# Kernel tuning notes

Measured on AMD Instinct MI355X. Metric: run time of the kernel, lower is better.

The kernel has to match this reference:

```python
import jax, jax.numpy as jnp
import numpy as np

# static multi-scale config (Deformable-DETR encoder, 1024x1024 image, strides 8/16/32/64)
SPATIAL_SHAPES = np.array([[128, 128], [64, 64], [32, 32], [16, 16]])  # (L, 2) = (h, w)
NUM_HEADS, NUM_LEVELS, NUM_POINTS = 8, 4, 4
EMBED, HEAD_DIM = 256, 32
NUM_KEYS = int(SPATIAL_SHAPES.prod(-1).sum())  # 21760


def _grid_sample(img, grid):
    """Bilinear grid_sample, padding_mode='zeros', align_corners=False.
    img: (BH, C, H, W); grid: (BH, Nq, P, 2) in [-1,1] -> (BH, C, Nq, P)."""
    BH, C, H, W = img.shape
    gx = (grid[..., 0] + 1.0) * (W / 2) - 0.5
    gy = (grid[..., 1] + 1.0) * (H / 2) - 0.5
    x0f, y0f = jnp.floor(gx), jnp.floor(gy)
    wx, wy = gx - x0f, gy - y0f
    x0, y0 = x0f.astype(jnp.int32), y0f.astype(jnp.int32)
    flat = img.reshape(BH, C, H * W)

    def gather(xi, yi, w):
        valid = (xi >= 0) & (xi < W) & (yi >= 0) & (yi < H)
        idx = jnp.clip(yi, 0, H - 1) * W + jnp.clip(xi, 0, W - 1)
        g = jnp.take_along_axis(flat, idx.reshape(BH, 1, -1), axis=2)
        g = g.reshape(BH, C, xi.shape[1], xi.shape[2])
        return g * (w * valid)[:, None]

    return (gather(x0, y0, (1 - wx) * (1 - wy)) + gather(x0 + 1, y0, wx * (1 - wy))
            + gather(x0, y0 + 1, (1 - wx) * wy) + gather(x0 + 1, y0 + 1, wx * wy))


def setup_inputs() -> dict:
    key = jax.random.key(0)
    ks = jax.random.split(key, 12)
    bs, nq = 1, NUM_KEYS
    s = 1.0 / np.sqrt(EMBED)
    return {
        "query": jax.random.normal(ks[0], (bs, nq, EMBED), jnp.float32),
        "query_pos": jax.random.normal(ks[1], (bs, nq, EMBED), jnp.float32),
        "value": jax.random.normal(ks[2], (bs, NUM_KEYS, EMBED), jnp.float32),
        "reference_points": jax.random.uniform(ks[3], (bs, nq, NUM_LEVELS, 2), jnp.float32),
        "spatial_shapes": jnp.asarray(SPATIAL_SHAPES, jnp.int32),
        "W_value": jax.random.normal(ks[4], (EMBED, EMBED), jnp.float32) * s,
        "b_value": jnp.zeros((EMBED,), jnp.float32),
        "W_off": jax.random.normal(ks[5], (NUM_HEADS * NUM_LEVELS * NUM_POINTS * 2, EMBED), jnp.float32) * 0.01,
        "b_off": jax.random.normal(ks[6], (NUM_HEADS * NUM_LEVELS * NUM_POINTS * 2,), jnp.float32),
        "W_attn": jax.random.normal(ks[7], (NUM_HEADS * NUM_LEVELS * NUM_POINTS, EMBED), jnp.float32) * s,
        "b_attn": jnp.zeros((NUM_HEADS * NUM_LEVELS * NUM_POINTS,), jnp.float32),
        "W_out": jax.random.normal(ks[8], (EMBED, EMBED), jnp.float32) * s,
        "b_out": jnp.zeros((EMBED,), jnp.float32),
    }


def reference(query, query_pos, value, reference_points, spatial_shapes,
              W_value, b_value, W_off, b_off, W_attn, b_attn, W_out, b_out):
    bs, nq, _ = query.shape
    identity = query
    q = query + query_pos  # pos_add
    v = value @ W_value.T + b_value  # value_proj: (bs, nk, E)
    v = v.reshape(bs, -1, NUM_HEADS, HEAD_DIM)

    offsets = (q @ W_off.T + b_off).reshape(bs, nq, NUM_HEADS, NUM_LEVELS, NUM_POINTS, 2)
    attn = (q @ W_attn.T + b_attn).reshape(bs, nq, NUM_HEADS, NUM_LEVELS * NUM_POINTS)
    attn = jax.nn.softmax(attn, axis=-1).reshape(bs, nq, NUM_HEADS, NUM_LEVELS, NUM_POINTS)

    # offset_normalizer = (w, h) per level; ref points are 2D -> loc = ref + off/norm
    normalizer = jnp.asarray(SPATIAL_SHAPES[:, ::-1].copy(), query.dtype)  # (L, 2)
    loc = reference_points[:, :, None, :, None, :] + offsets / normalizer[None, None, None, :, None, :]
    grids = 2.0 * loc - 1.0  # (bs, nq, H, L, P, 2)

    starts = np.concatenate([[0], np.cumsum(SPATIAL_SHAPES.prod(-1))])
    sampled = []
    for lvl in range(NUM_LEVELS):
        H_, W_ = int(SPATIAL_SHAPES[lvl, 0]), int(SPATIAL_SHAPES[lvl, 1])
        v_l = v[:, int(starts[lvl]):int(starts[lvl + 1])]  # (bs, H*W, heads, Dh)
        v_l = v_l.transpose(0, 2, 3, 1).reshape(bs * NUM_HEADS, HEAD_DIM, H_, W_)
        g_l = grids[:, :, :, lvl].transpose(0, 2, 1, 3, 4).reshape(bs * NUM_HEADS, nq, NUM_POINTS, 2)
        sampled.append(_grid_sample(v_l, g_l))  # (bs*H, Dh, nq, P)
    sampled = jnp.concatenate(sampled, axis=-1)  # (bs*H, Dh, nq, L*P)

    aw = attn.transpose(0, 2, 1, 3, 4).reshape(bs * NUM_HEADS, 1, nq, NUM_LEVELS * NUM_POINTS)
    out = (sampled * aw).sum(-1).reshape(bs, NUM_HEADS * HEAD_DIM, nq).transpose(0, 2, 1)
    out = out @ W_out.T + b_out  # output_proj
    return out + identity  # residual (dropout is identity at eval)
```

## Files before the change

kernel.cpp:

```cpp
#include <hip/hip_runtime.h>
#include <hip/hip_bf16.h>
#include <math.h>
#include <type_traits>

#define K_DIM 256
using bf16 = __hip_bfloat16;

typedef __attribute__((ext_vector_type(8))) short s8v;
typedef __attribute__((ext_vector_type(4))) float f4v;

__device__ __forceinline__ float b2f(unsigned short u) {
    return __uint_as_float(((unsigned)u) << 16);
}
__device__ __forceinline__ unsigned short f2b(float f) {
    unsigned u = __float_as_uint(f);
    unsigned r = 0x7FFFu + ((u >> 16) & 1u);
    return (unsigned short)((u + r) >> 16);
}
__device__ __forceinline__ float  ld1(const float* p) { return *p; }
__device__ __forceinline__ float  ld1(const bf16*  p) { return b2f(*(const unsigned short*)p); }
__device__ __forceinline__ void   st1(float* p, float v) { *p = v; }
__device__ __forceinline__ void   st1(bf16*  p, float v) { *(unsigned short*)p = f2b(v); }
__device__ __forceinline__ float4 ld4(const float* p) { return *(const float4*)p; }
__device__ __forceinline__ float4 ld4(const bf16*  p) {
    ushort4 u = *(const ushort4*)p;
    return make_float4(b2f(u.x), b2f(u.y), b2f(u.z), b2f(u.w));
}
__device__ __forceinline__ s8v ldw8(const bf16* p) { return *(const s8v*)p; }

__device__ __forceinline__ bool detect_bf16(const unsigned* __restrict__ qw) {
    unsigned w = qw[threadIdx.x & 63];
    unsigned t = (w >> 8) & 0x7F;
    bool hit = (t >= 0x3Bu) && (t <= 0x42u);
    unsigned long long m = __ballot(hit);
    return __popcll(m) >= 32;
}

#define P1_TOTAL 164480
__global__ __launch_bounds__(256) void k_prep1(
    const unsigned* __restrict__ qd,
    const void* wv, const void* wo, const void* wa,
    const void* bv, const void* bo, const void* ba, bf16* __restrict__ dst)
{
    const bool isb = detect_bf16(qd);
    const int i4 = (blockIdx.x * 256 + threadIdx.x) * 4;
    if (i4 >= P1_TOTAL) return;
    const void* src; int off;
    if      (i4 < 65536)  { src = wv; off = i4; }
    else if (i4 < 131072) { src = wo; off = i4 - 65536; }
    else if (i4 < 163840) { src = wa; off = i4 - 131072; }
    else if (i4 < 164096) { src = bv; off = i4 - 163840; }
    else if (i4 < 164352) { src = bo; off = i4 - 164096; }
    else                  { src = ba; off = i4 - 164352; }
    if (isb) {
        *(ushort4*)(dst + i4) = *(const ushort4*)((const unsigned short*)src + off);
    } else {
        float4 v = *(const float4*)((const float*)src + off);
        *(ushort4*)(dst + i4) = make_ushort4(f2b(v.x), f2b(v.y), f2b(v.z), f2b(v.w));
    }
}

#define P2_TOTAL 65792
__global__ __launch_bounds__(256) void k_prep2(
    const unsigned* __restrict__ qd,
    const void* wout, const void* bout, bf16* __restrict__ dst)
{
    const bool isb = detect_bf16(qd);
    const int i4 = (blockIdx.x * 256 + threadIdx.x) * 4;
    if (i4 >= P2_TOTAL) return;
    const void* src; int off;
    if (i4 < 65536) { src = wout; off = i4; }
    else            { src = bout; off = i4 - 65536; }
    if (isb) {
        *(ushort4*)(dst + i4) = *(const ushort4*)((const unsigned short*)src + off);
    } else {
        float4 v = *(const float4*)((const float*)src + off);
        *(ushort4*)(dst + i4) = make_ushort4(f2b(v.x), f2b(v.y), f2b(v.z), f2b(v.w));
    }
}

template<typename AT, typename RT, typename CT, int NFRAG, bool ADD_A2, bool SPLIT, bool ADD_RES, bool HMAJOR>
__device__ __forceinline__ void mfma_gemm_body(
    unsigned short* __restrict__ As,
    const AT* __restrict__ A1, const AT* __restrict__ A2,
    const bf16* __restrict__ W1, const bf16* __restrict__ bias1, CT* __restrict__ C1, int N1,
    const bf16* __restrict__ W2, const bf16* __restrict__ bias2, bf16* __restrict__ C2, int N2,
    const RT* __restrict__ Res, int Mtot)
{
    const int tid = threadIdx.x;
    const int bm = blockIdx.x * 32;

    {
        const AT* t1 = A1 + (size_t)bm * K_DIM;
        if constexpr (!ADD_A2 && std::is_same<AT, bf16>::value) {
            #pragma unroll
            for (int j = 0; j < 4; ++j) {
                const int e = j * 2048 + tid * 8;
                const int row = e >> 8, col = e & 255;
                *(s8v*)&As[row * 264 + col] = *(const s8v*)(t1 + e);
            }
        } else {
            const AT* t2 = ADD_A2 ? (A2 + (size_t)bm * K_DIM) : (const AT*)0;
            #pragma unroll
            for (int j = 0; j < 8; ++j) {
                const int e = j * 1024 + tid * 4;
                float4 v = ld4(t1 + e);
                if (ADD_A2) {
                    float4 w2 = ld4(t2 + e);
                    v.x += w2.x; v.y += w2.y; v.z += w2.z; v.w += w2.w;
                }
                const int row = e >> 8, col = e & 255;
                *(ushort4*)&As[row * 264 + col] =
                    make_ushort4(f2b(v.x), f2b(v.y), f2b(v.z), f2b(v.w));
            }
        }
    }
    __syncthreads();

    const int wv = tid >> 6;
    const int lane = tid & 63;
    const int n15 = lane & 15;
    const int quad = lane >> 4;

    const bf16* Wr[NFRAG];
    int col[NFRAG];
    #pragma unroll
    for (int f = 0; f < NFRAG; ++f) {
        const int c = (wv * NFRAG + f) * 16 + n15;
        col[f] = c;
        if (SPLIT && c >= N1) Wr[f] = W2 + (size_t)(c - N1) * K_DIM;
        else                  Wr[f] = W1 + (size_t)c * K_DIM;
    }

    const f4v zz = {0.f, 0.f, 0.f, 0.f};
    f4v acc[2][NFRAG];
    #pragma unroll
    for (int mi = 0; mi < 2; ++mi)
        #pragma unroll
        for (int f = 0; f < NFRAG; ++f) acc[mi][f] = zz;

    #pragma unroll
    for (int kk = 0; kk < 8; ++kk) {
        const int k0 = kk * 32 + quad * 8;
        s8v b[NFRAG];
        #pragma unroll
        for (int f = 0; f < NFRAG; ++f) b[f] = ldw8(Wr[f] + k0);
        s8v a[2];
        #pragma unroll
        for (int mi = 0; mi < 2; ++mi)
            a[mi] = *(const s8v*)&As[(mi * 16 + n15) * 264 + k0];
        #pragma unroll
        for (int mi = 0; mi < 2; ++mi)
            #pragma unroll
            for (int f = 0; f < NFRAG; ++f)
                acc[mi][f] = __builtin_amdgcn_mfma_f32_16x16x32_bf16(a[mi], b[f], acc[mi][f], 0, 0, 0);
    }

    #pragma unroll
    for (int f = 0; f < NFRAG; ++f) {
        const int c = col[f];
        const bool hi = SPLIT && (c >= N1);
        const float bv = hi ? ld1(bias2 + (c - N1)) : ld1(bias1 + c);
        size_t hbase = 0;
        if (HMAJOR) hbase = (size_t)(c >> 5) * (size_t)Mtot * 32 + (c & 31);
        #pragma unroll
        for (int mi = 0; mi < 2; ++mi)
            #pragma unroll
            for (int r = 0; r < 4; ++r) {
                const int m = bm + mi * 16 + quad * 4 + r;
                float v = acc[mi][f][r] + bv;
                if (ADD_RES) v += ld1(Res + (size_t)m * N1 + c);
                if (hi)          st1(C2 + (size_t)m * N2 + (c - N1), v);
                else if (HMAJOR) st1(C1 + hbase + (size_t)m * 32, v);
                else             st1(C1 + (size_t)m * N1 + c, v);
            }
    }
}

template<int NFRAG, bool ADD_A2, bool SPLIT, bool HMAJOR>
__global__ __launch_bounds__(256) void k_gemm(
    const unsigned* __restrict__ qd, const void* A1, const void* A2,
    const bf16* W1, const bf16* b1, bf16* C1, int N1,
    const bf16* W2, const bf16* b2, bf16* C2, int N2, int Mtot)
{
    __shared__ unsigned short As[32 * 264];
    if (detect_bf16(qd))
        mfma_gemm_body<bf16, float, bf16, NFRAG, ADD_A2, SPLIT, false, HMAJOR>(As,
            (const bf16*)A1, (const bf16*)A2, W1, b1, C1, N1, W2, b2, C2, N2, nullptr, Mtot);
    else
        mfma_gemm_body<float, float, bf16, NFRAG, ADD_A2, SPLIT, false, HMAJOR>(As,
            (const float*)A1, (const float*)A2, W1, b1, C1, N1, W2, b2, C2, N2, nullptr, Mtot);
}

__global__ __launch_bounds__(256) void k_gemm_final(
    const unsigned* __restrict__ qd, const bf16* A1,
    const bf16* W, const bf16* bias, const void* Res, void* C)
{
    __shared__ unsigned short As[32 * 264];
    if (detect_bf16(qd))
        mfma_gemm_body<bf16, bf16, bf16, 4, false, false, true, false>(As,
            A1, nullptr, W, bias, (bf16*)C, 256,
            nullptr, nullptr, nullptr, 0, (const bf16*)Res, 0);
    else
        mfma_gemm_body<bf16, float, float, 4, false, false, true, false>(As,
            A1, nullptr, W, bias, (float*)C, 256,
            nullptr, nullptr, nullptr, 0, (const float*)Res, 0);
}

struct SampLds {
    float    swgt[4][128][4];
    unsigned sidx[4][128][4];
};

__global__ __launch_bounds__(256) void k_sample(
    const unsigned* __restrict__ qd, const bf16* __restrict__ vproj,
    bf16* __restrict__ osb, const bf16* __restrict__ logits,
    const void* __restrict__ refp, int Mtot)
{
    __shared__ SampLds L;
    const bool isb = detect_bf16(qd);
    const int t = threadIdx.x;
    const int qg = t >> 6;
    const int t64 = t & 63;
    const int q = blockIdx.x * 4 + qg;

    float f0, f1, f2, f3;
    {
        ushort4 u = *(const ushort4*)(osb + (size_t)q * 256 + t64 * 4);
        f0 = b2f(u.x); f1 = b2f(u.y); f2 = b2f(u.z); f3 = b2f(u.w);
    }

    float p0, p1;
    {
        ushort2 lu = *(const ushort2*)(logits + (size_t)q * 128 + t64 * 2);
        float l0 = b2f(lu.x), l1 = b2f(lu.y);
        float mx = fmaxf(l0, l1);
        mx = fmaxf(mx, __shfl_xor(mx, 1));
        mx = fmaxf(mx, __shfl_xor(mx, 2));
        mx = fmaxf(mx, __shfl_xor(mx, 4));
        float e0 = __expf(l0 - mx), e1 = __expf(l1 - mx);
        float s = e0 + e1;
        s += __shfl_xor(s, 1);
        s += __shfl_xor(s, 2);
        s += __shfl_xor(s, 4);
        const float inv = 1.f / s;
        p0 = e0 * inv; p1 = e1 * inv;
    }

    const int hh  = t64 & 7;
    const int i2  = t64 >> 3;
    const int src = (hh << 3) | i2;
    const float o0 = __shfl(f0, src);
    const float o1 = __shfl(f1, src);
    const float o2 = __shfl(f2, src);
    const float o3 = __shfl(f3, src);
    const float pa = __shfl(p0, src);
    const float pb = __shfl(p1, src);

    const int lv = i2 >> 1;
    float rx, ry;
    if (isb) {
        rx = ld1((const bf16*)refp + (size_t)q * 8 + 2 * lv);
        ry = ld1((const bf16*)refp + (size_t)q * 8 + 2 * lv + 1);
    } else {
        rx = ld1((const float*)refp + (size_t)q * 8 + 2 * lv);
        ry = ld1((const float*)refp + (size_t)q * 8 + 2 * lv + 1);
    }

    #pragma unroll
    for (int tt = 0; tt < 2; ++tt) {
        const int i = i2 * 2 + tt;
        const int l = i >> 2;
        const int WW = 128 >> l;
        const int st = (l == 0) ? 0 : (l == 1) ? 16384 : (l == 2) ? 20480 : 21504;
        const float ox = tt ? o2 : o0;
        const float oy = tt ? o3 : o1;
        const float aw = tt ? pb : pa;
        const float gx = rx * (float)WW + ox - 0.5f;
        const float gy = ry * (float)WW + oy - 0.5f;
        const float x0f = floorf(gx);
        const float y0f = floorf(gy);
        const float wx = gx - x0f;
        const float wy = gy - y0f;
        const int x0 = (int)x0f;
        const int y0 = (int)y0f;
        const float vx0 = (x0 >= 0 && x0 < WW) ? 1.f : 0.f;
        const float vx1 = (x0 + 1 >= 0 && x0 + 1 < WW) ? 1.f : 0.f;
        const float vy0 = (y0 >= 0 && y0 < WW) ? 1.f : 0.f;
        const float vy1 = (y0 + 1 >= 0 && y0 + 1 < WW) ? 1.f : 0.f;
        const int xc0 = min(max(x0, 0), WW - 1);
        const int xc1 = min(max(x0 + 1, 0), WW - 1);
        const int yc0 = min(max(y0, 0), WW - 1);
        const int yc1 = min(max(y0 + 1, 0), WW - 1);
        const int slot = t64 + (tt << 6);
        *(float4*)L.swgt[qg][slot] = make_float4(
            (1.f - wx) * (1.f - wy) * aw * vx0 * vy0,
            wx * (1.f - wy) * aw * vx1 * vy0,
            (1.f - wx) * wy * aw * vx0 * vy1,
            wx * wy * aw * vx1 * vy1);
        *(uint4*)L.sidx[qg][slot] = make_uint4(
            (unsigned)(st + yc0 * WW + xc0) * 64u,
            (unsigned)(st + yc0 * WW + xc1) * 64u,
            (unsigned)(st + yc1 * WW + xc0) * 64u,
            (unsigned)(st + yc1 * WW + xc1) * 64u);
    }
    __syncthreads();

    const int h  = t64 >> 3;
    const int dg = t64 & 7;
    const unsigned hb = (unsigned)(h * Mtot) * 64u + (unsigned)dg * 8u;
    const char* vb = (const char*)vproj;
    float a0 = 0.f, a1 = 0.f, a2 = 0.f, a3 = 0.f;
    #pragma unroll
    for (int i = 0; i < 16; ++i) {
        const int slot = ((i >> 1) << 3) | h | ((i & 1) << 6);
        const uint4  iv = *(const uint4*)L.sidx[qg][slot];
        const float4 wv = *(const float4*)L.swgt[qg][slot];
        {
            ushort4 pv = *(const ushort4*)(vb + (size_t)(iv.x + hb));
            a0 = fmaf(wv.x, b2f(pv.x), a0); a1 = fmaf(wv.x, b2f(pv.y), a1);
            a2 = fmaf(wv.x, b2f(pv.z), a2); a3 = fmaf(wv.x, b2f(pv.w), a3);
        }
        {
            ushort4 pv = *(const ushort4*)(vb + (size_t)(iv.y + hb));
            a0 = fmaf(wv.y, b2f(pv.x), a0); a1 = fmaf(wv.y, b2f(pv.y), a1);
            a2 = fmaf(wv.y, b2f(pv.z), a2); a3 = fmaf(wv.y, b2f(pv.w), a3);
        }
        {
            ushort4 pv = *(const ushort4*)(vb + (size_t)(iv.z + hb));
            a0 = fmaf(wv.z, b2f(pv.x), a0); a1 = fmaf(wv.z, b2f(pv.y), a1);
            a2 = fmaf(wv.z, b2f(pv.z), a2); a3 = fmaf(wv.z, b2f(pv.w), a3);
        }
        {
            ushort4 pv = *(const ushort4*)(vb + (size_t)(iv.w + hb));
            a0 = fmaf(wv.w, b2f(pv.x), a0); a1 = fmaf(wv.w, b2f(pv.y), a1);
            a2 = fmaf(wv.w, b2f(pv.z), a2); a3 = fmaf(wv.w, b2f(pv.w), a3);
        }
    }
    *(ushort4*)(osb + (size_t)q * 256 + h * 32 + dg * 4) =
        make_ushort4(f2b(a0), f2b(a1), f2b(a2), f2b(a3));
}

extern "C" void kernel_launch(void* const* d_in, const int* in_sizes, int n_in,
                              void* d_out, int out_size, void* d_ws, size_t ws_size,
                              hipStream_t stream) {
    const void* query     = d_in[0];
    const void* query_pos = d_in[1];
    const void* value     = d_in[2];
    const void* refp      = d_in[3];
    const void* W_value = d_in[5];
    const void* b_value = d_in[6];
    const void* W_off   = d_in[7];
    const void* b_off   = d_in[8];
    const void* W_attn  = d_in[9];
    const void* b_attn  = d_in[10];
    const void* W_out   = d_in[11];
    const void* b_out   = d_in[12];
    const unsigned* qd = (const unsigned*)d_in[0];

    const int M = in_sizes[0] / 256;
    char* wsb = (char*)d_ws;

    bf16* vproj = (bf16*)wsb;
    bf16* osb   = (bf16*)(wsb + (size_t)M * 512);
    bf16* logit = (bf16*)d_out;
    bf16* wc1   = (bf16*)((char*)d_out + (8u << 20));
    const bf16* c_wv = wc1;
    const bf16* c_wo = wc1 + 65536;
    const bf16* c_wa = wc1 + 131072;
    const bf16* c_bv = wc1 + 163840;
    const bf16* c_bo = wc1 + 164096;
    const bf16* c_ba = wc1 + 164352;
    bf16* wc2 = vproj;

    dim3 blk(256, 1, 1);
    dim3 g32((unsigned)(M / 32), 1, 1);
    dim3 gs((unsigned)(M / 4), 1, 1);

    k_prep1<<<dim3((P1_TOTAL / 4 + 255) / 256), blk, 0, stream>>>(qd,
        W_value, W_off, W_attn, b_value, b_off, b_attn, wc1);
    k_gemm<4, false, false, true><<<g32, blk, 0, stream>>>(qd, value, nullptr,
        c_wv, c_bv, vproj, 256, nullptr, nullptr, nullptr, 0, M);
    k_gemm<6, true, true, false><<<g32, blk, 0, stream>>>(qd, query, query_pos,
        c_wo, c_bo, osb, 256, c_wa, c_ba, logit, 128, M);
    k_sample<<<gs, blk, 0, stream>>>(qd, vproj, osb, logit, refp, M);
    k_prep2<<<dim3((P2_TOTAL / 4 + 255) / 256), blk, 0, stream>>>(qd, W_out, b_out, wc2);
    k_gemm_final<<<g32, blk, 0, stream>>>(qd, osb, wc2, wc2 + 65536, query, d_out);
}
```

Baseline: 232.2 us.

## Store offsets, logits and sampled output head-major; assign one head per sampling block

The offset/attention GEMM now writes its outputs in head-major layout (offsets per head in 32-wide rows, logits in 16-wide rows). The sampling kernel is remapped so each block handles 32 queries of a single head, with each thread owning one query-point pair, which removes the cross-lane shuffles. The final GEMM reads the head-major sampled output. The intent is that all 32 queries in a block gather from the same head's value plane, improving cache locality in the bilinear gathers. The cost is strided 16-byte A-tile loads in the final GEMM and scattered stores in the offset GEMM epilogue.

```diff
diff --git a/kernel.cpp b/kernel.cpp
--- a/kernel.cpp
+++ b/kernel.cpp
@@ -79,7 +79,8 @@
     }
 }
 
-template<typename AT, typename RT, typename CT, int NFRAG, bool ADD_A2, bool SPLIT, bool ADD_RES, bool HMAJOR>
+template<typename AT, typename RT, typename CT, int NFRAG, bool ADD_A2, bool SPLIT,
+         bool ADD_RES, bool HMAJOR, bool HM2, bool A1HM>
 __device__ __forceinline__ void mfma_gemm_body(
     unsigned short* __restrict__ As,
     const AT* __restrict__ A1, const AT* __restrict__ A2,
@@ -97,7 +98,13 @@
             for (int j = 0; j < 4; ++j) {
                 const int e = j * 2048 + tid * 8;
                 const int row = e >> 8, col = e & 255;
-                *(s8v*)&As[row * 264 + col] = *(const s8v*)(t1 + e);
+                const bf16* src;
+                if constexpr (A1HM)
+                    src = (const bf16*)A1 +
+                          ((size_t)(col >> 5) * (size_t)Mtot + (size_t)(bm + row)) * 32 + (col & 31);
+                else
+                    src = t1 + e;
+                *(s8v*)&As[row * 264 + col] = *(const s8v*)src;
             }
         } else {
             const AT* t2 = ADD_A2 ? (A2 + (size_t)bm * K_DIM) : (const AT*)0;
@@ -160,9 +167,12 @@
     for (int f = 0; f < NFRAG; ++f) {
         const int c = col[f];
         const bool hi = SPLIT && (c >= N1);
-        const float bv = hi ? ld1(bias2 + (c - N1)) : ld1(bias1 + c);
+        const int cc = hi ? (c - N1) : c;
+        const float bv = hi ? ld1(bias2 + cc) : ld1(bias1 + c);
         size_t hbase = 0;
         if (HMAJOR) hbase = (size_t)(c >> 5) * (size_t)Mtot * 32 + (c & 31);
+        size_t hbase2 = 0;
+        if (HM2) hbase2 = (size_t)(cc >> 4) * (size_t)Mtot * 16 + (cc & 15);
         #pragma unroll
         for (int mi = 0; mi < 2; ++mi)
             #pragma unroll
@@ -170,14 +180,17 @@
                 const int m = bm + mi * 16 + quad * 4 + r;
                 float v = acc[mi][f][r] + bv;
                 if (ADD_RES) v += ld1(Res + (size_t)m * N1 + c);
-                if (hi)          st1(C2 + (size_t)m * N2 + (c - N1), v);
+                if (hi) {
+                    if (HM2) st1(C2 + hbase2 + (size_t)m * 16, v);
+                    else     st1(C2 + (size_t)m * N2 + cc, v);
+                }
                 else if (HMAJOR) st1(C1 + hbase + (size_t)m * 32, v);
                 else             st1(C1 + (size_t)m * N1 + c, v);
             }
     }
 }
 
-template<int NFRAG, bool ADD_A2, bool SPLIT, bool HMAJOR>
+template<int NFRAG, bool ADD_A2, bool SPLIT, bool HMAJOR, bool HM2>
 __global__ __launch_bounds__(256) void k_gemm(
     const unsigned* __restrict__ qd, const void* A1, const void* A2,
     const bf16* W1, const bf16* b1, bf16* C1, int N1,
@@ -185,31 +198,31 @@
 {
     __shared__ unsigned short As[32 * 264];
     if (detect_bf16(qd))
-        mfma_gemm_body<bf16, float, bf16, NFRAG, ADD_A2, SPLIT, false, HMAJOR>(As,
+        mfma_gemm_body<bf16, float, bf16, NFRAG, ADD_A2, SPLIT, false, HMAJOR, HM2, false>(As,
             (const bf16*)A1, (const bf16*)A2, W1, b1, C1, N1, W2, b2, C2, N2, nullptr, Mtot);
     else
-        mfma_gemm_body<float, float, bf16, NFRAG, ADD_A2, SPLIT, false, HMAJOR>(As,
+        mfma_gemm_body<float, float, bf16, NFRAG, ADD_A2, SPLIT, false, HMAJOR, HM2, false>(As,
             (const float*)A1, (const float*)A2, W1, b1, C1, N1, W2, b2, C2, N2, nullptr, Mtot);
 }
 
 __global__ __launch_bounds__(256) void k_gemm_final(
     const unsigned* __restrict__ qd, const bf16* A1,
-    const bf16* W, const bf16* bias, const void* Res, void* C)
+    const bf16* W, const bf16* bias, const void* Res, void* C, int Mtot)
 {
     __shared__ unsigned short As[32 * 264];
     if (detect_bf16(qd))
-        mfma_gemm_body<bf16, bf16, bf16, 4, false, false, true, false>(As,
+        mfma_gemm_body<bf16, bf16, bf16, 4, false, false, true, false, false, true>(As,
             A1, nullptr, W, bias, (bf16*)C, 256,
-            nullptr, nullptr, nullptr, 0, (const bf16*)Res, 0);
+            nullptr, nullptr, nullptr, 0, (const bf16*)Res, Mtot);
     else
-        mfma_gemm_body<bf16, float, float, 4, false, false, true, false>(As,
+        mfma_gemm_body<bf16, float, float, 4, false, false, true, false, false, true>(As,
             A1, nullptr, W, bias, (float*)C, 256,
-            nullptr, nullptr, nullptr, 0, (const float*)Res, 0);
+            nullptr, nullptr, nullptr, 0, (const float*)Res, Mtot);
 }
 
 struct SampLds {
-    float    swgt[4][128][4];
-    unsigned sidx[4][128][4];
+    float    swgt[16][32][4];
+    unsigned sidx[16][32][4];
 };
 
 __global__ __launch_bounds__(256) void k_sample(
@@ -219,20 +232,23 @@
 {
     __shared__ SampLds L;
     const bool isb = detect_bf16(qd);
-    const int t = threadIdx.x;
-    const int qg = t >> 6;
-    const int t64 = t & 63;
-    const int q = blockIdx.x * 4 + qg;
+    const int t  = threadIdx.x;
+    const int p  = t >> 3;
+    const int dg = t & 7;
+    const int head = blockIdx.x & 7;
+    const int qc   = blockIdx.x >> 3;
+    const int q = qc * 32 + p;
+    const size_t hm = (size_t)head * (size_t)Mtot;
 
     float f0, f1, f2, f3;
     {
-        ushort4 u = *(const ushort4*)(osb + (size_t)q * 256 + t64 * 4);
+        ushort4 u = *(const ushort4*)(osb + (hm + q) * 32 + dg * 4);
         f0 = b2f(u.x); f1 = b2f(u.y); f2 = b2f(u.z); f3 = b2f(u.w);
     }
 
     float p0, p1;
     {
-        ushort2 lu = *(const ushort2*)(logits + (size_t)q * 128 + t64 * 2);
+        ushort2 lu = *(const ushort2*)(logits + (hm + q) * 16 + dg * 2);
         float l0 = b2f(lu.x), l1 = b2f(lu.y);
         float mx = fmaxf(l0, l1);
         mx = fmaxf(mx, __shfl_xor(mx, 1));
@@ -247,17 +263,7 @@
         p0 = e0 * inv; p1 = e1 * inv;
     }
 
-    const int hh  = t64 & 7;
-    const int i2  = t64 >> 3;
-    const int src = (hh << 3) | i2;
-    const float o0 = __shfl(f0, src);
-    const float o1 = __shfl(f1, src);
-    const float o2 = __shfl(f2, src);
-    const float o3 = __shfl(f3, src);
-    const float pa = __shfl(p0, src);
-    const float pb = __shfl(p1, src);
-
-    const int lv = i2 >> 1;
+    const int lv = dg >> 1;
     float rx, ry;
     if (isb) {
         rx = ld1((const bf16*)refp + (size_t)q * 8 + 2 * lv);
@@ -269,13 +275,13 @@
 
     #pragma unroll
     for (int tt = 0; tt < 2; ++tt) {
-        const int i = i2 * 2 + tt;
+        const int i = dg * 2 + tt;
         const int l = i >> 2;
         const int WW = 128 >> l;
         const int st = (l == 0) ? 0 : (l == 1) ? 16384 : (l == 2) ? 20480 : 21504;
-        const float ox = tt ? o2 : o0;
-        const float oy = tt ? o3 : o1;
-        const float aw = tt ? pb : pa;
+        const float ox = tt ? f2 : f0;
+        const float oy = tt ? f3 : f1;
+        const float aw = tt ? p1 : p0;
         const float gx = rx * (float)WW + ox - 0.5f;
         const float gy = ry * (float)WW + oy - 0.5f;
         const float x0f = floorf(gx);
@@ -292,13 +298,12 @@
         const int xc1 = min(max(x0 + 1, 0), WW - 1);
         const int yc0 = min(max(y0, 0), WW - 1);
         const int yc1 = min(max(y0 + 1, 0), WW - 1);
-        const int slot = t64 + (tt << 6);
-        *(float4*)L.swgt[qg][slot] = make_float4(
+        *(float4*)L.swgt[i][p] = make_float4(
             (1.f - wx) * (1.f - wy) * aw * vx0 * vy0,
             wx * (1.f - wy) * aw * vx1 * vy0,
             (1.f - wx) * wy * aw * vx0 * vy1,
             wx * wy * aw * vx1 * vy1);
-        *(uint4*)L.sidx[qg][slot] = make_uint4(
+        *(uint4*)L.sidx[i][p] = make_uint4(
             (unsigned)(st + yc0 * WW + xc0) * 64u,
             (unsigned)(st + yc0 * WW + xc1) * 64u,
             (unsigned)(st + yc1 * WW + xc0) * 64u,
@@ -306,16 +311,13 @@
     }
     __syncthreads();
 
-    const int h  = t64 >> 3;
-    const int dg = t64 & 7;
-    const unsigned hb = (unsigned)(h * Mtot) * 64u + (unsigned)dg * 8u;
+    const unsigned hb = (unsigned)(hm * 64) + (unsigned)dg * 8u;
     const char* vb = (const char*)vproj;
     float a0 = 0.f, a1 = 0.f, a2 = 0.f, a3 = 0.f;
     #pragma unroll
     for (int i = 0; i < 16; ++i) {
-        const int slot = ((i >> 1) << 3) | h | ((i & 1) << 6);
-        const uint4  iv = *(const uint4*)L.sidx[qg][slot];
-        const float4 wv = *(const float4*)L.swgt[qg][slot];
+        const uint4  iv = *(const uint4*)L.sidx[i][p];
+        const float4 wv = *(const float4*)L.swgt[i][p];
         {
             ushort4 pv = *(const ushort4*)(vb + (size_t)(iv.x + hb));
             a0 = fmaf(wv.x, b2f(pv.x), a0); a1 = fmaf(wv.x, b2f(pv.y), a1);
@@ -337,7 +339,7 @@
             a2 = fmaf(wv.w, b2f(pv.z), a2); a3 = fmaf(wv.w, b2f(pv.w), a3);
         }
     }
-    *(ushort4*)(osb + (size_t)q * 256 + h * 32 + dg * 4) =
+    *(ushort4*)(osb + (hm + q) * 32 + dg * 4) =
         make_ushort4(f2b(a0), f2b(a1), f2b(a2), f2b(a3));
 }
 
@@ -379,11 +381,11 @@
 
     k_prep1<<<dim3((P1_TOTAL / 4 + 255) / 256), blk, 0, stream>>>(qd,
         W_value, W_off, W_attn, b_value, b_off, b_attn, wc1);
-    k_gemm<4, false, false, true><<<g32, blk, 0, stream>>>(qd, value, nullptr,
+    k_gemm<4, false, false, true, false><<<g32, blk, 0, stream>>>(qd, value, nullptr,
         c_wv, c_bv, vproj, 256, nullptr, nullptr, nullptr, 0, M);
-    k_gemm<6, true, true, false><<<g32, blk, 0, stream>>>(qd, query, query_pos,
+    k_gemm<6, true, true, true, true><<<g32, blk, 0, stream>>>(qd, query, query_pos,
         c_wo, c_bo, osb, 256, c_wa, c_ba, logit, 128, M);
     k_sample<<<gs, blk, 0, stream>>>(qd, vproj, osb, logit, refp, M);
     k_prep2<<<dim3((P2_TOTAL / 4 + 255) / 256), blk, 0, stream>>>(qd, W_out, b_out, wc2);
-    k_gemm_final<<<g32, blk, 0, stream>>>(qd, osb, wc2, wc2 + 65536, query, d_out);
-}
+    k_gemm_final<<<g32, blk, 0, stream>>>(qd, osb, wc2, wc2 + 65536, query, d_out, M);
+}
```

New measurement: 223.6 us. 1.04x faster.
